# Performance work log

Measured on AMD Instinct MI355X. Metric: run time of the kernel, lower is better.

The kernel has to match this reference:

```python
import jax, jax.numpy as jnp
import numpy as np

IDIM, CDIM, NUM_HEADS, N, M = 256, 512, 2, 128, 64
T, BSZ = 64, 128


def setup_inputs() -> dict:
    key = jax.random.key(0)
    ks = jax.random.split(key, 12)
    return {
        "embs": jax.random.normal(ks[0], (T, BSZ, IDIM), jnp.float32),
        "lens": jnp.clip(jax.random.randint(ks[1], (BSZ,), 0, 64), 1, T).astype(jnp.int32),
        "mem_bias": jax.random.normal(ks[2], (N, M), jnp.float32) * 0.05,
        "W_ih": jax.random.normal(ks[3], (4 * CDIM, IDIM + NUM_HEADS * M), jnp.float32) * 0.04,
        "W_hh": jax.random.normal(ks[4], (4 * CDIM, CDIM), jnp.float32) * 0.04,
        "b_ih": jnp.zeros((4 * CDIM,), jnp.float32),
        "b_hh": jnp.zeros((4 * CDIM,), jnp.float32),
        "Wr": jax.random.normal(ks[5], (NUM_HEADS, M + 6, CDIM), jnp.float32) * 0.04,
        "br": jnp.zeros((NUM_HEADS, M + 6), jnp.float32),
        "Ww": jax.random.normal(ks[6], (NUM_HEADS, 3 * M + 6, CDIM), jnp.float32) * 0.04,
        "bw": jnp.zeros((NUM_HEADS, 3 * M + 6), jnp.float32),
        "h0": jax.random.normal(ks[7], (CDIM,), jnp.float32) * 0.05,
        "c0": jax.random.normal(ks[8], (CDIM,), jnp.float32) * 0.05,
        "r0": jax.random.normal(ks[9], (NUM_HEADS, M), jnp.float32) * 0.02,
    }


def _address(mem, k, beta, g, s, gamma, w_prev):
    # mem: (b,N,M)  k:(b,M)  beta,g,gamma:(b,1)  s:(b,3)  w_prev:(b,N)
    beta = jax.nn.softplus(beta)
    g = jax.nn.sigmoid(g)
    s = jax.nn.softmax(s, axis=1)
    gamma = 1.0 + jax.nn.softplus(gamma)
    kk = k + 1e-16
    mm = mem + 1e-16
    dot = jnp.einsum('bnm,bm->bn', mm, kk)
    denom = jnp.linalg.norm(mm, axis=-1) * jnp.linalg.norm(kk, axis=-1, keepdims=True)
    sim = dot / jnp.maximum(denom, 1e-8)  # torch cosine_similarity eps
    wc = jax.nn.softmax(beta * sim, axis=1)
    wg = g * wc + (1.0 - g) * w_prev
    # circular convolution with 3-tap shift kernel: c[i]=s0*w[i-1]+s1*w[i]+s2*w[i+1]
    ww = (s[:, 0:1] * jnp.roll(wg, 1, axis=1)
          + s[:, 1:2] * wg
          + s[:, 2:3] * jnp.roll(wg, -1, axis=1))
    wp = ww ** gamma
    return wp / (jnp.sum(wp, axis=1, keepdims=True) + 1e-16)


def _split5(o):
    return o[:, :M], o[:, M:M + 1], o[:, M + 1:M + 2], o[:, M + 2:M + 5], o[:, M + 5:M + 6]


def _ntm_forward(embs, mem_bias, W_ih, W_hh, b_ih, b_hh, Wr, br, Ww, bw, h0, c0, r0):
    bsz = embs.shape[1]
    mem0 = jnp.broadcast_to(mem_bias, (bsz, N, M))
    reads0 = jnp.broadcast_to(r0[:, None, :], (NUM_HEADS, bsz, M))
    w0 = jnp.zeros((NUM_HEADS, bsz, N), embs.dtype)
    h = jnp.broadcast_to(h0, (bsz, CDIM))
    c = jnp.broadcast_to(c0, (bsz, CDIM))

    def step(carry, emb):
        h, c, mem, rw, wws, reads = carry
        x = jnp.concatenate([emb] + [reads[i] for i in range(NUM_HEADS)], axis=1)
        gates = x @ W_ih.T + h @ W_hh.T + (b_ih + b_hh)
        gi, gf, gg, go = jnp.split(gates, 4, axis=1)  # torch LSTM gate order i,f,g,o
        c = jax.nn.sigmoid(gf) * c + jax.nn.sigmoid(gi) * jnp.tanh(gg)
        h = jax.nn.sigmoid(go) * jnp.tanh(c)
        ctrl = h
        new_reads, new_rw, new_wws = [], [], []
        for hi in range(NUM_HEADS):  # head order: read_i then write_i, writes visible to later heads
            orh = ctrl @ Wr[hi].T + br[hi]
            k, beta, g, s, gamma = _split5(orh)
            w = _address(mem, k, beta, g, s, gamma, rw[hi])
            new_rw.append(w)
            new_reads.append(jnp.einsum('bn,bnm->bm', w, mem))
            owh = ctrl @ Ww[hi].T + bw[hi]
            k2, beta2, g2, s2, gamma2 = _split5(owh)
            e = jax.nn.sigmoid(owh[:, M + 6:2 * M + 6])
            a = owh[:, 2 * M + 6:3 * M + 6]
            w2 = _address(mem, k2, beta2, g2, s2, gamma2, wws[hi])
            mem = mem * (1.0 - w2[:, :, None] * e[:, None, :]) + w2[:, :, None] * a[:, None, :]
            new_wws.append(w2)
        o = jnp.concatenate([ctrl] + new_reads, axis=1)
        carry = (h, c, mem, jnp.stack(new_rw), jnp.stack(new_wws), jnp.stack(new_reads))
        return carry, (o, h, c)

    _, (os_, hs, cs) = jax.lax.scan(step, (h, c, mem0, w0, w0, reads0), embs)
    return os_, hs, cs  # (T,b,cdim+H*M), (T,b,cdim), (T,b,cdim)


def reference(embs, lens, mem_bias, W_ih, W_hh, b_ih, b_hh, Wr, br, Ww, bw, h0, c0, r0):
    os_, hs, cs = _ntm_forward(embs, mem_bias, W_ih, W_hh, b_ih, b_hh, Wr, br, Ww, bw, h0, c0, r0)
    bsz = embs.shape[1]
    bi = jnp.arange(bsz)
    h_fin = hs[lens - 1, bi][None]  # (1,b,cdim) final state at true sequence end
    c_fin = cs[lens - 1, bi][None]
    return os_, h_fin, c_fin
```

## Files before the change

### kernel.cpp

```cpp
#include <hip/hip_runtime.h>
#include <cmath>

#define WS_EMBT  0
#define WS_STATE 2097152
#define WS_C     2260992
#define WS_MEM   2326528
#define WS_RW    3375104
#define WS_WWS   3407872
#define WS_PART  3440640

#define GLD16(g, l) __builtin_amdgcn_global_load_lds( \
    (const __attribute__((address_space(1))) void*)(g), \
    (__attribute__((address_space(3))) void*)(l), 16, 0, 0)

__device__ __forceinline__ float sigm(float x) { return 1.0f / (1.0f + expf(-x)); }
__device__ __forceinline__ float softplusf(float x) {
    return fmaxf(x, 0.0f) + log1pf(expf(-fabsf(x)));
}

__global__ __launch_bounds__(256) void k_embT(const float* __restrict__ embs,
                                              float* __restrict__ ws)
{
    int f4 = blockIdx.x * 256 + threadIdx.x;
    int k4 = f4 & 63, b = (f4 >> 6) & 127, t = f4 >> 13;
    float4 v = *(const float4*)&embs[(size_t)(t * 128 + b) * 256 + k4 * 4];
    *(float4*)&ws[WS_EMBT + ((size_t)(t * 64 + k4) * 128 + b) * 4] = v;
}

__global__ __launch_bounds__(256) void k_init(float* __restrict__ ws,
                                              const float* __restrict__ mem_bias,
                                              const float* __restrict__ h0,
                                              const float* __restrict__ c0,
                                              const float* __restrict__ r0)
{
    int i = blockIdx.x * 256 + threadIdx.x;
    if (i < 81920) {
        int ks = i >> 9, c4 = i & 3;
        int k = ks * 4 + c4;
        ws[WS_STATE + i] = (ks < 32) ? r0[k] : h0[k - 128];
        return;
    }
    int j = i - 81920;
    if (j < 65536) { ws[WS_C + j] = c0[j & 511]; return; }
    j -= 65536;
    if (j < 1048576) { ws[WS_MEM + j] = mem_bias[j & 8191]; return; }
    j -= 1048576;
    ws[WS_RW + j] = 0.0f;
}

__device__ __forceinline__ void ka_issue_chunk(
    const float* __restrict__ embsT, const float* __restrict__ stateT,
    float4* __restrict__ xs4, int buf, int c, int tx, int wid, int half)
{
#pragma unroll
    for (int it = 0; it < 4; ++it) {
        int f = it * 256 + tx;
        if (it < 3 || tx < 128) {
            int k4g = c * 14 + (f >> 6);
            int b   = half * 64 + (f & 63);
            const float* gp = (k4g < 64)
                ? &embsT[(size_t)k4g * 512 + b * 4]
                : &stateT[(size_t)(k4g - 64) * 512 + b * 4];
            GLD16(gp, &xs4[buf * 896 + it * 256 + wid * 64]);
        }
    }
}

__global__ void __launch_bounds__(256) k_gates_lstm(
    const float* __restrict__ W_ih,
    const float* __restrict__ W_hh,
    const float* __restrict__ b_ih,
    const float* __restrict__ b_hh,
    float* __restrict__ ws,
    float* __restrict__ d_out,
    const int* __restrict__ lens,
    int t)
{
    __shared__ float xs[2 * 3584];
    __shared__ float gx[16 * 64];
    float4* xs4 = (float4*)xs;

    const int tx = threadIdx.x;
    const int ct = blockIdx.x & 127, half = blockIdx.x >> 7;
    const int ch0 = ct * 4;
    const int p0 = t & 1, p1 = p0 ^ 1;
    const int lane = tx & 63, wid = tx >> 6;

    const float* embsT  = ws + WS_EMBT + (size_t)t * 32768;
    const float* stateT = ws + WS_STATE + (size_t)p0 * 81920;

    const int chw = ch0 + __builtin_amdgcn_readfirstlane(wid);
    const float* pih0 = W_ih + (size_t)(0 * 512 + chw) * 384;
    const float* pih1 = W_ih + (size_t)(1 * 512 + chw) * 384;
    const float* pih2 = W_ih + (size_t)(2 * 512 + chw) * 384;
    const float* pih3 = W_ih + (size_t)(3 * 512 + chw) * 384;
    const float* phh0 = W_hh + (size_t)(0 * 512 + chw) * 512 - 384;
    const float* phh1 = W_hh + (size_t)(1 * 512 + chw) * 512 - 384;
    const float* phh2 = W_hh + (size_t)(2 * 512 + chw) * 512 - 384;
    const float* phh3 = W_hh + (size_t)(3 * 512 + chw) * 512 - 384;

    float acc0 = 0.f, acc1 = 0.f, acc2 = 0.f, acc3 = 0.f;

    ka_issue_chunk(embsT, stateT, xs4, 0, 0, tx, wid, half);
    int cur = 0;
    for (int c = 0; c < 16; ++c) {
        __syncthreads();
        if (c < 15)
            ka_issue_chunk(embsT, stateT, xs4, cur ^ 1, c + 1, tx, wid, half);
#pragma unroll
        for (int k4 = 0; k4 < 14; ++k4) {
            const int kg = c * 56 + k4 * 4;
            float4 xv = xs4[cur * 896 + k4 * 64 + lane];
            const bool ih = (kg < 384);
            float4 w0 = ih ? *(const float4*)&pih0[kg] : *(const float4*)&phh0[kg];
            float4 w1 = ih ? *(const float4*)&pih1[kg] : *(const float4*)&phh1[kg];
            float4 w2 = ih ? *(const float4*)&pih2[kg] : *(const float4*)&phh2[kg];
            float4 w3 = ih ? *(const float4*)&pih3[kg] : *(const float4*)&phh3[kg];
            acc0 += w0.x * xv.x + w0.y * xv.y + w0.z * xv.z + w0.w * xv.w;
            acc1 += w1.x * xv.x + w1.y * xv.y + w1.z * xv.z + w1.w * xv.w;
            acc2 += w2.x * xv.x + w2.y * xv.y + w2.z * xv.z + w2.w * xv.w;
            acc3 += w3.x * xv.x + w3.y * xv.y + w3.z * xv.z + w3.w * xv.w;
        }
        cur ^= 1;
    }

    gx[(wid * 4 + 0) * 64 + lane] = acc0;
    gx[(wid * 4 + 1) * 64 + lane] = acc1;
    gx[(wid * 4 + 2) * 64 + lane] = acc2;
    gx[(wid * 4 + 3) * 64 + lane] = acc3;
    __syncthreads();

    {
        int ch_l = tx & 3, b_loc = tx >> 2;
        int b = half * 64 + b_loc;
        int ch = ch0 + ch_l;
        float gi = gx[(ch_l * 4 + 0) * 64 + b_loc] + b_ih[0 * 512 + ch] + b_hh[0 * 512 + ch];
        float gf = gx[(ch_l * 4 + 1) * 64 + b_loc] + b_ih[1 * 512 + ch] + b_hh[1 * 512 + ch];
        float gg = gx[(ch_l * 4 + 2) * 64 + b_loc] + b_ih[2 * 512 + ch] + b_hh[2 * 512 + ch];
        float go = gx[(ch_l * 4 + 3) * 64 + b_loc] + b_ih[3 * 512 + ch] + b_hh[3 * 512 + ch];
        float* cp = ws + WS_C + b * 512 + ch;
        float c_old = *cp;
        float c_new = sigm(gf) * c_old + sigm(gi) * tanhf(gg);
        float h_new = sigm(go) * tanhf(c_new);
        *cp = c_new;
        ws[WS_STATE + (size_t)p1 * 81920 + (32 + ct) * 512 + b * 4 + ch_l] = h_new;
        d_out[((size_t)t * 128 + b) * 640 + ch] = h_new;
        if (lens[b] - 1 == t) {
            d_out[5242880 + b * 512 + ch] = h_new;
            d_out[5308416 + b * 512 + ch] = c_new;
        }
    }
}

__global__ __launch_bounds__(256) void k_proj(
    const float* __restrict__ ws_c,
    const float* __restrict__ Wr,
    const float* __restrict__ Ww,
    float* __restrict__ part2,
    int t)
{
    __shared__ float w_s[16 * 64];
    __shared__ float x_s[16 * 128 * 4];
    float4* w_s4 = (float4*)w_s;
    float4* x_s4 = (float4*)x_s;

    const int tx = threadIdx.x;
    const int jt = blockIdx.x >> 3, kz = blockIdx.x & 7;
    const int j0 = jt * 16, k0 = kz * 64;
    const float* stateT = ws_c + WS_STATE + (size_t)((t + 1) & 1) * 81920;

    {
        int rl = tx >> 4, kq = tx & 15;
        int j = j0 + rl;
        float4 v = make_float4(0.f, 0.f, 0.f, 0.f);
        if (j < 536) {
            int hi = j >= 268, q = j - hi * 268;
            v = (q < 70) ? *(const float4*)&Wr[(hi * 70 + q) * 512 + k0 + kq * 4]
                         : *(const float4*)&Ww[(hi * 198 + (q - 70)) * 512 + k0 + kq * 4];
        }
        w_s4[tx] = v;
    }
#pragma unroll
    for (int it = 0; it < 8; ++it) {
        int f = it * 256 + tx;
        int k4 = f >> 7, b = f & 127;
        x_s4[f] = *(const float4*)&stateT[(size_t)(32 + kz * 16 + k4) * 512 + b * 4];
    }
    __syncthreads();

    const int lane = tx & 63, wid = tx >> 6;
    const int jw0 = wid * 4;
    float acc0[4] = {}, acc1[4] = {};
#pragma unroll 4
    for (int k4 = 0; k4 < 16; ++k4) {
        float4 xv0 = x_s4[k4 * 128 + lane];
        float4 xv1 = x_s4[k4 * 128 + 64 + lane];
#pragma unroll
        for (int r = 0; r < 4; ++r) {
            float4 wv = w_s4[(jw0 + r) * 16 + k4];
            acc0[r] += wv.x * xv0.x + wv.y * xv0.y + wv.z * xv0.z + wv.w * xv0.w;
            acc1[r] += wv.x * xv1.x + wv.y * xv1.y + wv.z * xv1.z + wv.w * xv1.w;
        }
    }
#pragma unroll
    for (int r = 0; r < 4; ++r) {
        int j = j0 + jw0 + r;
        if (j < 536) {
            part2[(size_t)kz * 69632 + lane * 544 + j]        = acc0[r];
            part2[(size_t)kz * 69632 + (lane + 64) * 544 + j] = acc1[r];
        }
    }
}

__global__ __launch_bounds__(256) void k_memops(
    const float* __restrict__ part2,
    const float* __restrict__ br,
    const float* __restrict__ bw,
    float* __restrict__ ws,
    float* __restrict__ d_out,
    int t)
{
    const int b = blockIdx.x;
    const int tx = threadIdx.x;
    const int lx = tx & 127;
    const int grp = tx >> 7;
    const int wid = tx >> 6;

    __shared__ float mem_s[128 * 66];
    __shared__ float proj_s[544];
    __shared__ float wg2_s[2 * 128];
    __shared__ float wf_s[2 * 128];
    __shared__ float red_s[16];
    __shared__ float ea_s[128];
    __shared__ float rvp_s[4 * 66];

    float* memg   = ws + WS_MEM;
    float* stateT = ws + WS_STATE + (size_t)((t + 1) & 1) * 81920;
    float* rwg    = ws + WS_RW;
    float* wwsg   = ws + WS_WWS;

    for (int j = tx; j < 536; j += 256) {
        int hi = j >= 268, q = j - hi * 268;
        float s = (q < 70) ? br[hi * 70 + q] : bw[hi * 198 + (q - 70)];
#pragma unroll
        for (int kzq = 0; kzq < 8; ++kzq)
            s += part2[(size_t)kzq * 69632 + b * 544 + j];
        proj_s[j] = s;
    }
#pragma unroll
    for (int e = 0; e < 8; ++e) {
        int f4 = e * 256 + tx;
        int n = f4 >> 4, m4 = (f4 & 15) * 4;
        float4 v = *(const float4*)&memg[b * 8192 + f4 * 4];
        *(float2*)&mem_s[n * 66 + m4]     = make_float2(v.x, v.y);
        *(float2*)&mem_s[n * 66 + m4 + 2] = make_float2(v.z, v.w);
    }
    __syncthreads();

    for (int hi = 0; hi < 2; ++hi) {
        const float* p = proj_s + hi * 268 + grp * 70;
        float* wprev_g = (grp == 0 ? rwg : wwsg) + (hi * 128 + b) * 128;

        float beta = softplusf(p[64]);
        float g = sigm(p[65]);
        float s0 = p[66], s1 = p[67], s2 = p[68];
        float sm = fmaxf(s0, fmaxf(s1, s2));
        float e0 = expf(s0 - sm), e1 = expf(s1 - sm), e2 = expf(s2 - sm);
        float sden = e0 + e1 + e2;
        s0 = e0 / sden; s1 = e1 / sden; s2 = e2 / sden;
        float gamma = 1.0f + softplusf(p[69]);

        const float* mrow = mem_s + lx * 66;
        float dot = 0.f, nm = 0.f, nk = 0.f;
#pragma unroll
        for (int m = 0; m < 64; m += 2) {
            float2 kv2 = *(const float2*)&p[m];
            float2 mv2 = *(const float2*)&mrow[m];
            float kx = kv2.x + 1e-16f, ky = kv2.y + 1e-16f;
            float mx = mv2.x + 1e-16f, my = mv2.y + 1e-16f;
            dot += mx * kx + my * ky;
            nm  += mx * mx + my * my;
            nk  += kx * kx + ky * ky;
        }
        float sim = dot / fmaxf(sqrtf(nm) * sqrtf(nk), 1e-8f);
        float z = beta * sim;

        float r = z;
#pragma unroll
        for (int d = 32; d > 0; d >>= 1) r = fmaxf(r, __shfl_xor(r, d));
        if ((tx & 63) == 0) red_s[wid] = r;
        __syncthreads();
        float zmax = fmaxf(red_s[grp * 2], red_s[grp * 2 + 1]);
        float ez = expf(z - zmax);
        r = ez;
#pragma unroll
        for (int d = 32; d > 0; d >>= 1) r += __shfl_xor(r, d);
        if ((tx & 63) == 0) red_s[8 + wid] = r;
        __syncthreads();
        float zsum = red_s[8 + grp * 2] + red_s[8 + grp * 2 + 1];
        float wc = ez / zsum;
        float wgv = g * wc + (1.f - g) * wprev_g[lx];
        wg2_s[grp * 128 + lx] = wgv;
        __syncthreads();
        float wwv = s0 * wg2_s[grp * 128 + ((lx + 127) & 127)] + s1 * wgv
                  + s2 * wg2_s[grp * 128 + ((lx + 1) & 127)];
        float wp = powf(wwv, gamma);
        r = wp;
#pragma unroll
        for (int d = 32; d > 0; d >>= 1) r += __shfl_xor(r, d);
        if ((tx & 63) == 0) red_s[wid] = r;
        __syncthreads();
        float psum = red_s[grp * 2] + red_s[grp * 2 + 1];
        float wfin = wp / (psum + 1e-16f);
        wf_s[grp * 128 + lx] = wfin;
        wprev_g[lx] = wfin;
        __syncthreads();

        {
            int m = tx & 63, p4 = tx >> 6;
            float rv = 0.f;
            const int nb = p4 * 32;
#pragma unroll
            for (int n8 = 0; n8 < 32; ++n8) {
                int n = nb + n8;
                rv += wf_s[n] * mem_s[n * 66 + m];
            }
            rvp_s[p4 * 66 + m] = rv;
        }
        if (tx < 64)        ea_s[tx] = sigm(proj_s[hi * 268 + 140 + tx]);
        else if (tx < 128)  ea_s[tx] = proj_s[hi * 268 + 204 + (tx - 64)];
        __syncthreads();

        if (tx < 64) {
            float rvf = rvp_s[tx] + rvp_s[66 + tx] + rvp_s[132 + tx] + rvp_s[198 + tx];
            stateT[((hi * 64 + tx) >> 2) * 512 + b * 4 + (tx & 3)] = rvf;
            d_out[((size_t)t * 128 + b) * 640 + 512 + hi * 64 + tx] = rvf;
        }
#pragma unroll
        for (int e = 0; e < 16; ++e) {
            int f = e * 256 + tx;
            int n = f >> 5, m2 = (f & 31) * 2;
            float w2 = wf_s[128 + n];
            float2 mv = *(const float2*)&mem_s[n * 66 + m2];
            mv.x = mv.x * (1.f - w2 * ea_s[m2])     + w2 * ea_s[64 + m2];
            mv.y = mv.y * (1.f - w2 * ea_s[m2 + 1]) + w2 * ea_s[65 + m2];
            *(float2*)&mem_s[n * 66 + m2] = mv;
            if (hi == 1) *(float2*)&memg[b * 8192 + f * 2] = mv;
        }
        __syncthreads();
    }
}

extern "C" void kernel_launch(void* const* d_in, const int* in_sizes, int n_in,
                              void* d_out, int out_size, void* d_ws, size_t ws_size,
                              hipStream_t stream)
{
    (void)in_sizes; (void)n_in; (void)out_size; (void)ws_size;
    const float* embs     = (const float*)d_in[0];
    const int*   lens     = (const int*)  d_in[1];
    const float* mem_bias = (const float*)d_in[2];
    const float* W_ih     = (const float*)d_in[3];
    const float* W_hh     = (const float*)d_in[4];
    const float* b_ih     = (const float*)d_in[5];
    const float* b_hh     = (const float*)d_in[6];
    const float* Wr       = (const float*)d_in[7];
    const float* br       = (const float*)d_in[8];
    const float* Ww       = (const float*)d_in[9];
    const float* bw       = (const float*)d_in[10];
    const float* h0       = (const float*)d_in[11];
    const float* c0       = (const float*)d_in[12];
    const float* r0       = (const float*)d_in[13];
    float* out = (float*)d_out;
    float* ws  = (float*)d_ws;
    float* part2 = ws + WS_PART;

    k_embT<<<2048, 256, 0, stream>>>(embs, ws);
    k_init<<<4928, 256, 0, stream>>>(ws, mem_bias, h0, c0, r0);
    for (int t = 0; t < 64; ++t) {
        k_gates_lstm<<<256, 256, 0, stream>>>(W_ih, W_hh, b_ih, b_hh,
                                              ws, out, lens, t);
        k_proj<<<272, 256, 0, stream>>>(ws, Wr, Ww, part2, t);
        k_memops<<<128, 256, 0, stream>>>(part2, br, bw, ws, out, t);
    }
}
```

Baseline: 3.279 ms.

## Stage LSTM gate weights through LDS with async loads and larger K chunks

The gates kernel now copies its 16 weight rows per K-chunk into shared memory with global_load_lds, double-buffered alongside the input activations. Previously each wave read weights straight from global memory inside the inner loop. The K chunk is doubled (8 chunks of 112 instead of 16 of 56) to halve barrier count, and dynamic shared memory of about 76KB is requested, with launch bounds hinting 2 blocks per CU. The aim is to take global-load latency off the FMA loop, at the cost of more LDS per block and possibly lower occupancy.

```diff
diff --git a/kernel.cpp b/kernel.cpp
--- a/kernel.cpp
+++ b/kernel.cpp
@@ -9,6 +9,9 @@
 #define WS_WWS   3407872
 #define WS_PART  3440640
 
+#define KA_LDS_FLOATS (3584 + 14336 + 1024)
+#define KA_LDS_BYTES  (KA_LDS_FLOATS * 4)
+
 #define GLD16(g, l) __builtin_amdgcn_global_load_lds( \
     (const __attribute__((address_space(1))) void*)(g), \
     (__attribute__((address_space(3))) void*)(l), 16, 0, 0)
@@ -48,25 +51,36 @@
     ws[WS_RW + j] = 0.0f;
 }
 
-__device__ __forceinline__ void ka_issue_chunk(
+__device__ __forceinline__ void ka_issue(
+    const float* __restrict__ W_ih, const float* __restrict__ W_hh,
     const float* __restrict__ embsT, const float* __restrict__ stateT,
-    float4* __restrict__ xs4, int buf, int c, int tx, int wid, int half)
-{
-#pragma unroll
-    for (int it = 0; it < 4; ++it) {
+    float4* __restrict__ w4, float4* __restrict__ x4,
+    int buf, int c, int tx, int wid, int half, int ch0)
+{
+#pragma unroll
+    for (int it = 0; it < 2; ++it) {
         int f = it * 256 + tx;
-        if (it < 3 || tx < 128) {
-            int k4g = c * 14 + (f >> 6);
-            int b   = half * 64 + (f & 63);
-            const float* gp = (k4g < 64)
-                ? &embsT[(size_t)k4g * 512 + b * 4]
-                : &stateT[(size_t)(k4g - 64) * 512 + b * 4];
-            GLD16(gp, &xs4[buf * 896 + it * 256 + wid * 64]);
-        }
-    }
-}
-
-__global__ void __launch_bounds__(256) k_gates_lstm(
+        if (it == 0 || tx < 192) {
+            int lr = f / 28, kq = f - lr * 28;
+            int grow = (lr & 3) * 512 + ch0 + (lr >> 2);
+            int kg = c * 112 + kq * 4;
+            const float* gp = (kg < 384) ? &W_ih[(size_t)grow * 384 + kg]
+                                         : &W_hh[(size_t)grow * 512 + kg - 384];
+            GLD16(gp, &w4[buf * 448 + it * 256 + wid * 64]);
+        }
+    }
+#pragma unroll
+    for (int it = 0; it < 7; ++it) {
+        int f = it * 256 + tx;
+        int k4g = c * 28 + (f >> 6);
+        int b = half * 64 + (f & 63);
+        const float* gp = (k4g < 64) ? &embsT[(size_t)k4g * 512 + b * 4]
+                                     : &stateT[(size_t)(k4g - 64) * 512 + b * 4];
+        GLD16(gp, &x4[buf * 1792 + it * 256 + wid * 64]);
+    }
+}
+
+__global__ void __launch_bounds__(256, 2) k_gates_lstm(
     const float* __restrict__ W_ih,
     const float* __restrict__ W_hh,
     const float* __restrict__ b_ih,
@@ -76,9 +90,10 @@
     const int* __restrict__ lens,
     int t)
 {
-    __shared__ float xs[2 * 3584];
-    __shared__ float gx[16 * 64];
-    float4* xs4 = (float4*)xs;
+    extern __shared__ float sm[];
+    float4* w4 = (float4*)sm;
+    float4* x4 = (float4*)(sm + 3584);
+    float*  gx = sm + 17920;
 
     const int tx = threadIdx.x;
     const int ct = blockIdx.x & 127, half = blockIdx.x >> 7;
@@ -89,33 +104,24 @@
     const float* embsT  = ws + WS_EMBT + (size_t)t * 32768;
     const float* stateT = ws + WS_STATE + (size_t)p0 * 81920;
 
-    const int chw = ch0 + __builtin_amdgcn_readfirstlane(wid);
-    const float* pih0 = W_ih + (size_t)(0 * 512 + chw) * 384;
-    const float* pih1 = W_ih + (size_t)(1 * 512 + chw) * 384;
-    const float* pih2 = W_ih + (size_t)(2 * 512 + chw) * 384;
-    const float* pih3 = W_ih + (size_t)(3 * 512 + chw) * 384;
-    const float* phh0 = W_hh + (size_t)(0 * 512 + chw) * 512 - 384;
-    const float* phh1 = W_hh + (size_t)(1 * 512 + chw) * 512 - 384;
-    const float* phh2 = W_hh + (size_t)(2 * 512 + chw) * 512 - 384;
-    const float* phh3 = W_hh + (size_t)(3 * 512 + chw) * 512 - 384;
-
     float acc0 = 0.f, acc1 = 0.f, acc2 = 0.f, acc3 = 0.f;
 
-    ka_issue_chunk(embsT, stateT, xs4, 0, 0, tx, wid, half);
+    ka_issue(W_ih, W_hh, embsT, stateT, w4, x4, 0, 0, tx, wid, half, ch0);
     int cur = 0;
-    for (int c = 0; c < 16; ++c) {
-        __syncthreads();
-        if (c < 15)
-            ka_issue_chunk(embsT, stateT, xs4, cur ^ 1, c + 1, tx, wid, half);
-#pragma unroll
-        for (int k4 = 0; k4 < 14; ++k4) {
-            const int kg = c * 56 + k4 * 4;
-            float4 xv = xs4[cur * 896 + k4 * 64 + lane];
-            const bool ih = (kg < 384);
-            float4 w0 = ih ? *(const float4*)&pih0[kg] : *(const float4*)&phh0[kg];
-            float4 w1 = ih ? *(const float4*)&pih1[kg] : *(const float4*)&phh1[kg];
-            float4 w2 = ih ? *(const float4*)&pih2[kg] : *(const float4*)&phh2[kg];
-            float4 w3 = ih ? *(const float4*)&pih3[kg] : *(const float4*)&phh3[kg];
+    for (int c = 0; c < 8; ++c) {
+        __syncthreads();
+        if (c < 7)
+            ka_issue(W_ih, W_hh, embsT, stateT, w4, x4, cur ^ 1, c + 1,
+                     tx, wid, half, ch0);
+        const float4* xb = x4 + cur * 1792;
+        const float4* wb = w4 + cur * 448 + wid * 4 * 28;
+#pragma unroll 4
+        for (int k4 = 0; k4 < 28; ++k4) {
+            float4 xv = xb[k4 * 64 + lane];
+            float4 w0 = wb[k4];
+            float4 w1 = wb[28 + k4];
+            float4 w2 = wb[56 + k4];
+            float4 w3 = wb[84 + k4];
             acc0 += w0.x * xv.x + w0.y * xv.y + w0.z * xv.z + w0.w * xv.w;
             acc1 += w1.x * xv.x + w1.y * xv.y + w1.z * xv.z + w1.w * xv.w;
             acc2 += w2.x * xv.x + w2.y * xv.y + w2.z * xv.z + w2.w * xv.w;
@@ -374,11 +380,14 @@
     float* ws  = (float*)d_ws;
     float* part2 = ws + WS_PART;
 
+    hipFuncSetAttribute(reinterpret_cast<const void*>(&k_gates_lstm),
+                        hipFuncAttributeMaxDynamicSharedMemorySize, KA_LDS_BYTES);
+
     k_embT<<<2048, 256, 0, stream>>>(embs, ws);
     k_init<<<4928, 256, 0, stream>>>(ws, mem_bias, h0, c0, r0);
     for (int t = 0; t < 64; ++t) {
-        k_gates_lstm<<<256, 256, 0, stream>>>(W_ih, W_hh, b_ih, b_hh,
-                                              ws, out, lens, t);
+        k_gates_lstm<<<256, 256, KA_LDS_BYTES, stream>>>(W_ih, W_hh, b_ih, b_hh,
+                                                         ws, out, lens, t);
         k_proj<<<272, 256, 0, stream>>>(ws, Wr, Ww, part2, t);
         k_memops<<<128, 256, 0, stream>>>(part2, br, bw, ws, out, t);
     }
```

New measurement: 3.573 ms. 1.09x slower.
